# Kernel tuning notes

Hardware: AMD Instinct MI355X
Metric: run time of the kernel (lower is better)

Reference implementation:

```python
import jax, jax.numpy as jnp
import numpy as np


def gcn_conv(x, W, b, src, dst, n_nodes):
    """PyG GCNConv: add self-loops, symmetric deg^-1/2 normalization,
    linear transform, scatter-add aggregation, bias."""
    loops = jnp.arange(n_nodes, dtype=src.dtype)
    s = jnp.concatenate([src, loops])  # sources (incl. self-loops)
    d = jnp.concatenate([dst, loops])  # targets
    deg = jax.ops.segment_sum(jnp.ones_like(d, dtype=x.dtype), d, num_segments=n_nodes)
    dinv = jnp.where(deg > 0, jax.lax.rsqrt(deg), 0.0)
    norm = dinv[s] * dinv[d]  # [E+N]
    h = x @ W  # [N, out]
    msg = h[s] * norm[:, None]  # [E+N, out]
    out = jax.ops.segment_sum(msg, d, num_segments=n_nodes)
    return out + b


def setup_inputs() -> dict:
    key = jax.random.key(0)
    ks = jax.random.split(key, 8)
    N, E, D, H = 50000, 600000, 128, 128
    x = jax.random.normal(ks[0], (N, D), dtype=jnp.float32)
    edge_index = jax.random.randint(ks[1], (2, E), 0, N, dtype=jnp.int64)
    sd = lambda fi: 1.0 / np.sqrt(fi)
    W1 = jax.random.normal(ks[2], (D, H), dtype=jnp.float32) * sd(D)
    b1 = jnp.zeros((H,), dtype=jnp.float32)
    W2 = jax.random.normal(ks[3], (H, H), dtype=jnp.float32) * sd(H)
    b2 = jnp.zeros((H,), dtype=jnp.float32)
    Wd = jax.random.normal(ks[4], (H, D), dtype=jnp.float32) * sd(H)
    bd = jnp.zeros((D,), dtype=jnp.float32)
    return {"x": x, "edge_index": edge_index, "W1": W1, "b1": b1,
            "W2": W2, "b2": b2, "Wd": Wd, "bd": bd}


def reference(x, edge_index, W1, b1, W2, b2, Wd, bd):
    n_nodes = x.shape[0]
    src, dst = edge_index[0], edge_index[1]
    h = gcn_conv(x, W1, b1, src, dst, n_nodes)
    h = jax.nn.relu(h)
    h = gcn_conv(h, W2, b2, src, dst, n_nodes)
    out = jax.nn.relu(h @ Wd + bd)  # decoder: Linear + ReLU
    return out
```

## Files before the change

### kernel.cpp

```cpp
#include <hip/hip_runtime.h>

typedef long long i64;
typedef __attribute__((ext_vector_type(8))) short short8;
typedef __attribute__((ext_vector_type(8))) unsigned short us8;
typedef __attribute__((ext_vector_type(4))) float f32x4;

#define DEG_STRIDE 64

__device__ __forceinline__ unsigned short bf16_rtn(float x) {
  unsigned u = __float_as_uint(x);
  unsigned r = (u + 0x7FFFu + ((u >> 16) & 1u)) >> 16;
  return (unsigned short)r;
}
__device__ __forceinline__ float bf16_to_f(unsigned short h) {
  return __uint_as_float(((unsigned)h) << 16);
}

__device__ __forceinline__ bool wave_is64(const int* __restrict__ ei32, i64 e0) {
  int probe = ei32[2 * e0 + 1];
  return __ballot(probe != 0) == 0ULL;
}

__global__ __launch_bounds__(256) void init_all_kernel(
    int* __restrict__ cnt, int N,
    const float* __restrict__ Wa, unsigned short* __restrict__ wha, unsigned short* __restrict__ wla,
    const float* __restrict__ Wb, unsigned short* __restrict__ whb, unsigned short* __restrict__ wlb,
    const float* __restrict__ Wc, unsigned short* __restrict__ whc, unsigned short* __restrict__ wlc,
    const int* __restrict__ ei32, int E, int* __restrict__ s32, int* __restrict__ d32) {
  int nbInit = (N + 255) >> 8;
  int bid = blockIdx.x;
  if (bid < nbInit) {
    int i = bid * 256 + threadIdx.x;
    if (i < N) cnt[i] = 0;
    return;
  }
  bid -= nbInit;
  if (bid < 192) {
    int b = bid >> 6;
    int t = (bid & 63) * 256 + threadIdx.x;
    const float* W = (b == 0) ? Wa : (b == 1) ? Wb : Wc;
    unsigned short* wh = (b == 0) ? wha : (b == 1) ? whb : whc;
    unsigned short* wl = (b == 0) ? wla : (b == 1) ? wlb : wlc;
    int c = t >> 7, k = t & 127;
    float w = W[k * 128 + c];
    unsigned short hi = bf16_rtn(w);
    unsigned short lo = bf16_rtn(w - bf16_to_f(hi));
    wh[c * 128 + k] = hi;
    wl[c * 128 + k] = lo;
    return;
  }
  bid -= 192;
  int e = bid * 256 + threadIdx.x;
  if (e >= E) return;
  bool is64 = wave_is64(ei32, e);
  s32[e] = is64 ? ei32[2 * (i64)e] : ei32[e];
  d32[e] = is64 ? ei32[2 * ((i64)E + e)] : ei32[(i64)E + e];
}

__global__ __launch_bounds__(256) void fill_kernel(const int* __restrict__ s32,
                                                   const int* __restrict__ d32,
                                                   int* __restrict__ cnt,
                                                   int* __restrict__ col, int E, int N) {
  int shard = blockIdx.x & 3;
  int chunk = blockIdx.x >> 2;
  int ns = (N + 3) >> 2;
  int lo = shard * ns, hi = min(lo + ns, N);
  int base = chunk * 2048;
  int t = threadIdx.x;
#pragma unroll
  for (int j = 0; j < 8; ++j) {
    int e = base + j * 256 + t;
    if (e >= E) break;
    int d = d32[e];
    if (d >= lo && d < hi) {
      int pos = atomicAdd(&cnt[d], 1);
      if (pos < DEG_STRIDE) col[(i64)d * DEG_STRIDE + pos] = s32[e];
    }
  }
}

template <int ABF16, int OUT>
__global__ __launch_bounds__(256, 2) void gemm_mfma(
    const void* __restrict__ Av, const unsigned short* __restrict__ WhT,
    const unsigned short* __restrict__ WlT, const float* __restrict__ bias,
    const int* __restrict__ cnt, void* __restrict__ outv, int N) {
  int tid = threadIdx.x;
  int wid = tid >> 6, lane = tid & 63;
  int lr = lane & 15, kg = (lane >> 4) * 8;
  int rowbase = blockIdx.x * 128 + wid * 32;

  f32x4 acc[2][8];
#pragma unroll
  for (int tr = 0; tr < 2; ++tr)
#pragma unroll
    for (int tc = 0; tc < 8; ++tc) acc[tr][tc] = (f32x4){0.f, 0.f, 0.f, 0.f};

  int r[2] = {rowbase + lr, rowbase + 16 + lr};

  for (int kc = 0; kc < 128; kc += 32) {
    int k0 = kc + kg;
    short8 afh[2], afl[2];
#pragma unroll
    for (int tr = 0; tr < 2; ++tr) {
      if (ABF16) {
        const unsigned short* Ab = (const unsigned short*)Av;
        us8 v = {0, 0, 0, 0, 0, 0, 0, 0};
        if (r[tr] < N) v = *reinterpret_cast<const us8*>(&Ab[(i64)r[tr] * 128 + k0]);
#pragma unroll
        for (int j = 0; j < 8; ++j) afh[tr][j] = (short)v[j];
      } else {
        const float* A = (const float*)Av;
        float4 va = make_float4(0.f, 0.f, 0.f, 0.f), vb = va;
        if (r[tr] < N) {
          const float* p = &A[(i64)r[tr] * 128 + k0];
          va = *reinterpret_cast<const float4*>(p);
          vb = *reinterpret_cast<const float4*>(p + 4);
        }
        float xs[8] = {va.x, va.y, va.z, va.w, vb.x, vb.y, vb.z, vb.w};
#pragma unroll
        for (int j = 0; j < 8; ++j) {
          unsigned short h = bf16_rtn(xs[j]);
          afh[tr][j] = (short)h;
          afl[tr][j] = (short)bf16_rtn(xs[j] - bf16_to_f(h));
        }
      }
    }
#pragma unroll
    for (int tc = 0; tc < 8; ++tc) {
      int c = tc * 16 + lr;
      short8 bfh = *reinterpret_cast<const short8*>(&WhT[c * 128 + k0]);
      short8 bfl = *reinterpret_cast<const short8*>(&WlT[c * 128 + k0]);
#pragma unroll
      for (int tr = 0; tr < 2; ++tr) {
        acc[tr][tc] = __builtin_amdgcn_mfma_f32_16x16x32_bf16(afh[tr], bfh, acc[tr][tc], 0, 0, 0);
        acc[tr][tc] = __builtin_amdgcn_mfma_f32_16x16x32_bf16(afh[tr], bfl, acc[tr][tc], 0, 0, 0);
        if (!ABF16)
          acc[tr][tc] = __builtin_amdgcn_mfma_f32_16x16x32_bf16(afl[tr], bfh, acc[tr][tc], 0, 0, 0);
      }
    }
  }

  if (OUT == 0) {
    unsigned short* hb = (unsigned short*)outv;
#pragma unroll
    for (int tr = 0; tr < 2; ++tr) {
#pragma unroll
      for (int reg = 0; reg < 4; ++reg) {
        int row = rowbase + tr * 16 + (lane >> 4) * 4 + reg;
        if (row >= N) continue;
        float dv = rsqrtf((float)cnt[row] + 1.0f);
#pragma unroll
        for (int tc = 0; tc < 8; ++tc) {
          int colg = tc * 16 + lr;
          hb[(i64)row * 128 + colg] = bf16_rtn(acc[tr][tc][reg] * dv);
        }
      }
    }
  } else {
    float* out = (float*)outv;
#pragma unroll
    for (int tr = 0; tr < 2; ++tr) {
#pragma unroll
      for (int reg = 0; reg < 4; ++reg) {
        int row = rowbase + tr * 16 + (lane >> 4) * 4 + reg;
        if (row >= N) continue;
#pragma unroll
        for (int tc = 0; tc < 8; ++tc) {
          int colg = tc * 16 + lr;
          float v = fmaxf(acc[tr][tc][reg] + bias[colg], 0.f);
          __builtin_nontemporal_store(v, &out[(i64)row * 128 + colg]);
        }
      }
    }
  }
}

template <int RELU>
__global__ __launch_bounds__(256) void agg_bf16(
    const unsigned short* __restrict__ hb, const int* __restrict__ col,
    const int* __restrict__ cnt, const float* __restrict__ bias,
    unsigned short* __restrict__ zout, int N) {
  int t = threadIdx.x;
  int lane = t & 63;
  int v = blockIdx.x * 16 + ((t >> 6) << 2) + (lane >> 4);
  int cl = lane & 15;
  if (v >= N) return;
  i64 base = (i64)v * 128 + cl * 8;
  us8 sv = *reinterpret_cast<const us8*>(&hb[base]);
  float a[8];
#pragma unroll
  for (int j = 0; j < 8; ++j) a[j] = bf16_to_f(sv[j]);

  int n = cnt[v];
  int end = min(n, DEG_STRIDE);
  const int* bucket = &col[(i64)v * DEG_STRIDE];
  int i = 0;
  for (; i + 7 < end; i += 8) {
    us8 u[8];
#pragma unroll
    for (int q = 0; q < 8; ++q)
      u[q] = *reinterpret_cast<const us8*>(&hb[(i64)bucket[i + q] * 128 + cl * 8]);
#pragma unroll
    for (int j = 0; j < 8; ++j)
      a[j] += ((bf16_to_f(u[0][j]) + bf16_to_f(u[1][j])) + (bf16_to_f(u[2][j]) + bf16_to_f(u[3][j]))) +
              ((bf16_to_f(u[4][j]) + bf16_to_f(u[5][j])) + (bf16_to_f(u[6][j]) + bf16_to_f(u[7][j])));
  }
  if (i + 3 < end) {
    us8 u[4];
#pragma unroll
    for (int q = 0; q < 4; ++q)
      u[q] = *reinterpret_cast<const us8*>(&hb[(i64)bucket[i + q] * 128 + cl * 8]);
#pragma unroll
    for (int j = 0; j < 8; ++j)
      a[j] += (bf16_to_f(u[0][j]) + bf16_to_f(u[1][j])) + (bf16_to_f(u[2][j]) + bf16_to_f(u[3][j]));
    i += 4;
  }
  for (; i < end; ++i) {
    us8 u0 = *reinterpret_cast<const us8*>(&hb[(i64)bucket[i] * 128 + cl * 8]);
#pragma unroll
    for (int j = 0; j < 8; ++j) a[j] += bf16_to_f(u0[j]);
  }

  float dv = rsqrtf((float)n + 1.0f);
  f32x4 b0 = *reinterpret_cast<const f32x4*>(&bias[cl * 8]);
  f32x4 b1 = *reinterpret_cast<const f32x4*>(&bias[cl * 8 + 4]);
  float rbias[8] = {b0[0], b0[1], b0[2], b0[3], b1[0], b1[1], b1[2], b1[3]};
  us8 o;
#pragma unroll
  for (int j = 0; j < 8; ++j) {
    float r = fmaf(a[j], dv, rbias[j]);
    if (RELU) r = fmaxf(r, 0.f);
    o[j] = bf16_rtn(r);
  }
  __builtin_nontemporal_store(o, reinterpret_cast<us8*>(&zout[base]));
}

extern "C" void kernel_launch(void* const* d_in, const int* in_sizes, int n_in,
                              void* d_out, int out_size, void* d_ws, size_t ws_size,
                              hipStream_t stream) {
  const float* x  = (const float*)d_in[0];
  const int*   ei = (const int*)d_in[1];
  const float* W1 = (const float*)d_in[2];
  const float* b1 = (const float*)d_in[3];
  const float* W2 = (const float*)d_in[4];
  const float* b2 = (const float*)d_in[5];
  const float* Wd = (const float*)d_in[6];
  const float* bd = (const float*)d_in[7];
  int N = in_sizes[0] / 128;
  int E = in_sizes[1] / 2;
  float* out = (float*)d_out;

  char* w = (char*)d_ws;
  unsigned short* zb   = (unsigned short*)w;
  unsigned short* wh1  = zb + (i64)N * 128;
  unsigned short* wl1  = wh1 + 16384;
  unsigned short* wh2  = wl1 + 16384;
  unsigned short* wl2  = wh2 + 16384;
  unsigned short* whd  = wl2 + 16384;
  unsigned short* wld  = whd + 16384;
  int*   cnt    = (int*)(wld + 16384);
  int*   col    = cnt + N;
  int*   s32    = col + (i64)N * DEG_STRIDE;
  int*   d32    = s32 + E;
  unsigned short* hb = (unsigned short*)d_out;

  int nbInit = (N + 255) / 256;
  int nbE = (E + 255) / 256;
  int cb = (E + 2047) / 2048;
  int gblocks = (N + 127) / 128;
  int ablocks = (N + 15) / 16;

  init_all_kernel<<<nbInit + 192 + nbE, 256, 0, stream>>>(cnt, N,
      W1, wh1, wl1, W2, wh2, wl2, Wd, whd, wld, ei, E, s32, d32);
  fill_kernel<<<4 * cb, 256, 0, stream>>>(s32, d32, cnt, col, E, N);

  gemm_mfma<0, 0><<<gblocks, 256, 0, stream>>>(x, wh1, wl1, nullptr, cnt, hb, N);
  agg_bf16<1><<<ablocks, 256, 0, stream>>>(hb, col, cnt, b1, zb, N);
  gemm_mfma<1, 0><<<gblocks, 256, 0, stream>>>(zb, wh2, wl2, nullptr, cnt, hb, N);
  agg_bf16<0><<<ablocks, 256, 0, stream>>>(hb, col, cnt, b2, zb, N);
  gemm_mfma<1, 1><<<gblocks, 256, 0, stream>>>(zb, whd, wld, bd, cnt, out, N);
}
```

Baseline: 164.7 us.

## Fuse CSR fill with first GEMM and move source degree scaling into aggregation

```diff
diff --git a/kernel.cpp b/kernel.cpp
--- a/kernel.cpp
+++ b/kernel.cpp
@@ -57,37 +57,14 @@
   d32[e] = is64 ? ei32[2 * ((i64)E + e)] : ei32[(i64)E + e];
 }
 
-__global__ __launch_bounds__(256) void fill_kernel(const int* __restrict__ s32,
-                                                   const int* __restrict__ d32,
-                                                   int* __restrict__ cnt,
-                                                   int* __restrict__ col, int E, int N) {
-  int shard = blockIdx.x & 3;
-  int chunk = blockIdx.x >> 2;
-  int ns = (N + 3) >> 2;
-  int lo = shard * ns, hi = min(lo + ns, N);
-  int base = chunk * 2048;
-  int t = threadIdx.x;
-#pragma unroll
-  for (int j = 0; j < 8; ++j) {
-    int e = base + j * 256 + t;
-    if (e >= E) break;
-    int d = d32[e];
-    if (d >= lo && d < hi) {
-      int pos = atomicAdd(&cnt[d], 1);
-      if (pos < DEG_STRIDE) col[(i64)d * DEG_STRIDE + pos] = s32[e];
-    }
-  }
-}
-
-template <int ABF16, int OUT>
-__global__ __launch_bounds__(256, 2) void gemm_mfma(
-    const void* __restrict__ Av, const unsigned short* __restrict__ WhT,
+template <int ABF16, int OUT, int SCALE>
+__device__ __forceinline__ void gemm_core(
+    int bid, int tid, const void* __restrict__ Av, const unsigned short* __restrict__ WhT,
     const unsigned short* __restrict__ WlT, const float* __restrict__ bias,
     const int* __restrict__ cnt, void* __restrict__ outv, int N) {
-  int tid = threadIdx.x;
   int wid = tid >> 6, lane = tid & 63;
   int lr = lane & 15, kg = (lane >> 4) * 8;
-  int rowbase = blockIdx.x * 128 + wid * 32;
+  int rowbase = bid * 128 + wid * 32;
 
   f32x4 acc[2][8];
 #pragma unroll
@@ -148,7 +125,7 @@
       for (int reg = 0; reg < 4; ++reg) {
         int row = rowbase + tr * 16 + (lane >> 4) * 4 + reg;
         if (row >= N) continue;
-        float dv = rsqrtf((float)cnt[row] + 1.0f);
+        float dv = SCALE ? rsqrtf((float)cnt[row] + 1.0f) : 1.0f;
 #pragma unroll
         for (int tc = 0; tc < 8; ++tc) {
           int colg = tc * 16 + lr;
@@ -175,7 +152,43 @@
   }
 }
 
-template <int RELU>
+template <int ABF16, int OUT>
+__global__ __launch_bounds__(256, 2) void gemm_mfma(
+    const void* __restrict__ Av, const unsigned short* __restrict__ WhT,
+    const unsigned short* __restrict__ WlT, const float* __restrict__ bias,
+    const int* __restrict__ cnt, void* __restrict__ outv, int N) {
+  gemm_core<ABF16, OUT, 1>(blockIdx.x, threadIdx.x, Av, WhT, WlT, bias, cnt, outv, N);
+}
+
+__global__ __launch_bounds__(256, 2) void fill_gemm1_kernel(
+    const int* __restrict__ s32, const int* __restrict__ d32,
+    int* __restrict__ cnt, int* __restrict__ col, int E, int N, int fillBlocks,
+    const float* __restrict__ x, const unsigned short* __restrict__ wh1,
+    const unsigned short* __restrict__ wl1, unsigned short* __restrict__ hb) {
+  if ((int)blockIdx.x >= fillBlocks) {
+    gemm_core<0, 0, 0>(blockIdx.x - fillBlocks, threadIdx.x, x, wh1, wl1,
+                       nullptr, nullptr, hb, N);
+    return;
+  }
+  int shard = blockIdx.x & 3;
+  int chunk = blockIdx.x >> 2;
+  int ns = (N + 3) >> 2;
+  int lo = shard * ns, hi = min(lo + ns, N);
+  int base = chunk * 2048;
+  int t = threadIdx.x;
+#pragma unroll
+  for (int j = 0; j < 8; ++j) {
+    int e = base + j * 256 + t;
+    if (e >= E) break;
+    int d = d32[e];
+    if (d >= lo && d < hi) {
+      int pos = atomicAdd(&cnt[d], 1);
+      if (pos < DEG_STRIDE) col[(i64)d * DEG_STRIDE + pos] = s32[e];
+    }
+  }
+}
+
+template <int RELU, int SRCSCALE>
 __global__ __launch_bounds__(256) void agg_bf16(
     const unsigned short* __restrict__ hb, const int* __restrict__ col,
     const int* __restrict__ cnt, const float* __restrict__ bias,
@@ -185,50 +198,78 @@
   int v = blockIdx.x * 16 + ((t >> 6) << 2) + (lane >> 4);
   int cl = lane & 15;
   if (v >= N) return;
+  int n = cnt[v];
+  float dvv = rsqrtf((float)n + 1.0f);
   i64 base = (i64)v * 128 + cl * 8;
   us8 sv = *reinterpret_cast<const us8*>(&hb[base]);
   float a[8];
 #pragma unroll
-  for (int j = 0; j < 8; ++j) a[j] = bf16_to_f(sv[j]);
-
-  int n = cnt[v];
+  for (int j = 0; j < 8; ++j)
+    a[j] = SRCSCALE ? dvv * bf16_to_f(sv[j]) : bf16_to_f(sv[j]);
+
   int end = min(n, DEG_STRIDE);
   const int* bucket = &col[(i64)v * DEG_STRIDE];
   int i = 0;
   for (; i + 7 < end; i += 8) {
+    int sq[8];
+#pragma unroll
+    for (int q = 0; q < 8; ++q) sq[q] = bucket[i + q];
     us8 u[8];
-#pragma unroll
-    for (int q = 0; q < 8; ++q)
-      u[q] = *reinterpret_cast<const us8*>(&hb[(i64)bucket[i + q] * 128 + cl * 8]);
+    float dvs[8];
+#pragma unroll
+    for (int q = 0; q < 8; ++q) {
+      u[q] = *reinterpret_cast<const us8*>(&hb[(i64)sq[q] * 128 + cl * 8]);
+      if (SRCSCALE) dvs[q] = rsqrtf((float)cnt[sq[q]] + 1.0f);
+    }
+#pragma unroll
+    for (int j = 0; j < 8; ++j) {
+      if (SRCSCALE) {
+#pragma unroll
+        for (int q = 0; q < 8; ++q) a[j] = fmaf(dvs[q], bf16_to_f(u[q][j]), a[j]);
+      } else {
+        a[j] += ((bf16_to_f(u[0][j]) + bf16_to_f(u[1][j])) + (bf16_to_f(u[2][j]) + bf16_to_f(u[3][j]))) +
+                ((bf16_to_f(u[4][j]) + bf16_to_f(u[5][j])) + (bf16_to_f(u[6][j]) + bf16_to_f(u[7][j])));
+      }
+    }
+  }
+  if (i + 3 < end) {
+    int sq[4];
+#pragma unroll
+    for (int q = 0; q < 4; ++q) sq[q] = bucket[i + q];
+    us8 u[4];
+    float dvs[4];
+#pragma unroll
+    for (int q = 0; q < 4; ++q) {
+      u[q] = *reinterpret_cast<const us8*>(&hb[(i64)sq[q] * 128 + cl * 8]);
+      if (SRCSCALE) dvs[q] = rsqrtf((float)cnt[sq[q]] + 1.0f);
+    }
+#pragma unroll
+    for (int j = 0; j < 8; ++j) {
+      if (SRCSCALE) {
+#pragma unroll
+        for (int q = 0; q < 4; ++q) a[j] = fmaf(dvs[q], bf16_to_f(u[q][j]), a[j]);
+      } else {
+        a[j] += (bf16_to_f(u[0][j]) + bf16_to_f(u[1][j])) + (bf16_to_f(u[2][j]) + bf16_to_f(u[3][j]));
+      }
+    }
+    i += 4;
+  }
+  for (; i < end; ++i) {
+    int s0 = bucket[i];
+    us8 u0 = *reinterpret_cast<const us8*>(&hb[(i64)s0 * 128 + cl * 8]);
+    float dvs0 = SRCSCALE ? rsqrtf((float)cnt[s0] + 1.0f) : 1.0f;
 #pragma unroll
     for (int j = 0; j < 8; ++j)
-      a[j] += ((bf16_to_f(u[0][j]) + bf16_to_f(u[1][j])) + (bf16_to_f(u[2][j]) + bf16_to_f(u[3][j]))) +
-              ((bf16_to_f(u[4][j]) + bf16_to_f(u[5][j])) + (bf16_to_f(u[6][j]) + bf16_to_f(u[7][j])));
-  }
-  if (i + 3 < end) {
-    us8 u[4];
-#pragma unroll
-    for (int q = 0; q < 4; ++q)
-      u[q] = *reinterpret_cast<const us8*>(&hb[(i64)bucket[i + q] * 128 + cl * 8]);
-#pragma unroll
-    for (int j = 0; j < 8; ++j)
-      a[j] += (bf16_to_f(u[0][j]) + bf16_to_f(u[1][j])) + (bf16_to_f(u[2][j]) + bf16_to_f(u[3][j]));
-    i += 4;
-  }
-  for (; i < end; ++i) {
-    us8 u0 = *reinterpret_cast<const us8*>(&hb[(i64)bucket[i] * 128 + cl * 8]);
-#pragma unroll
-    for (int j = 0; j < 8; ++j) a[j] += bf16_to_f(u0[j]);
-  }
-
-  float dv = rsqrtf((float)n + 1.0f);
+      a[j] = SRCSCALE ? fmaf(dvs0, bf16_to_f(u0[j]), a[j]) : (a[j] + bf16_to_f(u0[j]));
+  }
+
   f32x4 b0 = *reinterpret_cast<const f32x4*>(&bias[cl * 8]);
   f32x4 b1 = *reinterpret_cast<const f32x4*>(&bias[cl * 8 + 4]);
   float rbias[8] = {b0[0], b0[1], b0[2], b0[3], b1[0], b1[1], b1[2], b1[3]};
   us8 o;
 #pragma unroll
   for (int j = 0; j < 8; ++j) {
-    float r = fmaf(a[j], dv, rbias[j]);
+    float r = fmaf(a[j], dvv, rbias[j]);
     if (RELU) r = fmaxf(r, 0.f);
     o[j] = bf16_rtn(r);
   }
@@ -272,11 +313,10 @@
 
   init_all_kernel<<<nbInit + 192 + nbE, 256, 0, stream>>>(cnt, N,
       W1, wh1, wl1, W2, wh2, wl2, Wd, whd, wld, ei, E, s32, d32);
-  fill_kernel<<<4 * cb, 256, 0, stream>>>(s32, d32, cnt, col, E, N);
-
-  gemm_mfma<0, 0><<<gblocks, 256, 0, stream>>>(x, wh1, wl1, nullptr, cnt, hb, N);
-  agg_bf16<1><<<ablocks, 256, 0, stream>>>(hb, col, cnt, b1, zb, N);
+  fill_gemm1_kernel<<<4 * cb + gblocks, 256, 0, stream>>>(
+      s32, d32, cnt, col, E, N, 4 * cb, x, wh1, wl1, hb);
+  agg_bf16<1, 1><<<ablocks, 256, 0, stream>>>(hb, col, cnt, b1, zb, N);
   gemm_mfma<1, 0><<<gblocks, 256, 0, stream>>>(zb, wh2, wl2, nullptr, cnt, hb, N);
-  agg_bf16<0><<<ablocks, 256, 0, stream>>>(hb, col, cnt, b2, zb, N);
+  agg_bf16<0, 0><<<ablocks, 256, 0, stream>>>(hb, col, cnt, b2, zb, N);
   gemm_mfma<1, 1><<<gblocks, 256, 0, stream>>>(zb, whd, wld, bd, cnt, out, N);
 }
```

Result: no change. 163.4 us (-0.8%).
